# Performance work log

Measured on AMD Instinct MI355X. Metric: run time of the kernel, lower is better.

The kernel has to match this reference:

```python
import jax, jax.numpy as jnp
import numpy as np

N_NODES = 100000
N_EDGES = 800000
HIDDEN = 256
BOTTLENECK = 32


def setup_inputs() -> dict:
    key = jax.random.key(0)
    k1, k2, k3, k4 = jax.random.split(key, 4)
    x = jax.random.normal(k1, (N_NODES, HIDDEN), dtype=jnp.float32)
    edge_index = jax.random.randint(k2, (2, N_EDGES), 0, N_NODES, dtype=jnp.int64)
    # PyG GCNConv linear weights, init per module: normal(std=1e-5), zero bias
    W_down = jax.random.normal(k3, (BOTTLENECK, HIDDEN), dtype=jnp.float32) * 1e-5
    b_down = jnp.zeros((BOTTLENECK,), dtype=jnp.float32)
    W_up = jax.random.normal(k4, (HIDDEN, BOTTLENECK), dtype=jnp.float32) * 1e-5
    b_up = jnp.zeros((HIDDEN,), dtype=jnp.float32)
    return {"x": x, "edge_index": edge_index, "W_down": W_down, "b_down": b_down,
            "W_up": W_up, "b_up": b_up}


def reference(x, edge_index, W_down, b_down, W_up, b_up):
    N = x.shape[0]
    loops = jnp.arange(N, dtype=edge_index.dtype)
    # gcn_norm with self-loops (edge weight = 1), symmetric normalization
    row = jnp.concatenate([edge_index[0], loops])  # source nodes
    col = jnp.concatenate([edge_index[1], loops])  # target nodes
    deg = jax.ops.segment_sum(jnp.ones(row.shape[0], dtype=x.dtype), col, num_segments=N)
    dinv = jnp.where(deg > 0, jax.lax.rsqrt(deg), 0.0)
    norm = dinv[row] * dinv[col]  # [E+N]

    def gcn_conv(h, W, b):
        h = h @ W.T                                   # [N, out]
        msgs = h[row] * norm[:, None]                 # gather + weight
        return jax.ops.segment_sum(msgs, col, num_segments=N) + b

    h = jax.nn.relu(gcn_conv(x, W_down, b_down))      # down-proj conv + act
    out = gcn_conv(h, W_up, b_up) + x                 # up-proj conv + skip
    return out
```

## Files before the change

kernel.cpp:

```cpp
#include <hip/hip_runtime.h>
#include <hip/hip_bf16.h>
#include <stdint.h>

#define HID 256
#define BOT 32

typedef short short8 __attribute__((ext_vector_type(8)));
typedef unsigned short ushort8 __attribute__((ext_vector_type(8)));
typedef float floatx4 __attribute__((ext_vector_type(4)));

__device__ __forceinline__ unsigned short f2bu(float f) {
    return (unsigned short)(__float_as_uint(f) >> 16);
}
__device__ __forceinline__ float bu2f(unsigned short u) {
    return __uint_as_float((unsigned int)u << 16);
}
__device__ __forceinline__ short8 pack8(float4 a, float4 b) {
    short8 r;
    r[0] = (short)f2bu(a.x); r[1] = (short)f2bu(a.y);
    r[2] = (short)f2bu(a.z); r[3] = (short)f2bu(a.w);
    r[4] = (short)f2bu(b.x); r[5] = (short)f2bu(b.y);
    r[6] = (short)f2bu(b.z); r[7] = (short)f2bu(b.w);
    return r;
}


__global__ void k_detect(const int* __restrict__ ei, int* __restrict__ flags) {
    int t = threadIdx.x;
    int found = 0;
    for (int i = 0; i < 8; ++i) {
        int slot = 2 * (t * 8 + i) + 1;
        if (ei[slot] != 0) found = 1;
    }
    unsigned long long b = __ballot(found);
    if (t == 0) flags[0] = (b == 0ULL) ? 1 : 0;
}

__global__ void k_deg(const int* __restrict__ ei, int E, int* __restrict__ deg,
                      const int* __restrict__ flags) {
    int mode = flags[0];
    int e = blockIdx.x * blockDim.x + threadIdx.x;
    if (e >= E) return;
    int d = mode ? ei[2 * E + 2 * e] : ei[E + e];
    atomicAdd(deg + d, 1);
}

__global__ __launch_bounds__(256) void k_alloc(const int* __restrict__ deg,
                                               float* __restrict__ dinv,
                                               int* __restrict__ start,
                                               int* __restrict__ cur,
                                               int* __restrict__ cursor, int N) {
    __shared__ int sdata[256];
    __shared__ int sbase;
    int tid = threadIdx.x;
    int i = blockIdx.x * 256 + tid;
    int d = (i < N) ? deg[i] : 0;
    if (i < N) dinv[i] = rsqrtf((float)(d + 1));
    sdata[tid] = d;
    __syncthreads();
    for (int off = 1; off < 256; off <<= 1) {
        int t = (tid >= off) ? sdata[tid - off] : 0;
        __syncthreads();
        sdata[tid] += t;
        __syncthreads();
    }
    if (tid == 0) sbase = atomicAdd(cursor, sdata[255]);
    __syncthreads();
    if (i < N) {
        int st = sbase + sdata[tid] - d;
        start[i] = st;
        cur[i] = st;
    }
}

__global__ void k_fill(const int* __restrict__ ei, int E,
                       const float* __restrict__ dinv,
                       int* __restrict__ cur, int2* __restrict__ srcw,
                       const int* __restrict__ flags) {
    int mode = flags[0];
    int e = blockIdx.x * blockDim.x + threadIdx.x;
    if (e >= E) return;
    int s, d;
    if (mode) { s = ei[2 * e]; d = ei[2 * E + 2 * e]; }
    else      { s = ei[e];     d = ei[E + e]; }
    float w = dinv[s] * dinv[d];
    int slot = atomicAdd(cur + d, 1);
    srcw[slot] = make_int2(s, __float_as_int(w));
}

__global__ __launch_bounds__(256) void k_gemm_down(
    const float* __restrict__ x, const float* __restrict__ Wd,
    unsigned short* __restrict__ P, int N, int nwaves)
{
    int wid  = (blockIdx.x * 256 + threadIdx.x) >> 6;
    int lane = threadIdx.x & 63;
    int m = lane & 15, q = lane >> 4;

    short8 bfr[2][8];
    #pragma unroll
    for (int jt = 0; jt < 2; ++jt) {
        const float4* wr = (const float4*)(Wd + (size_t)(jt * 16 + m) * HID);
        #pragma unroll
        for (int ks = 0; ks < 8; ++ks) {
            int c = (ks * 32 + q * 8) >> 2;
            bfr[jt][ks] = pack8(wr[c], wr[c + 1]);
        }
    }

    int tiles = (N + 15) >> 4;
    for (int t = wid; t < tiles; t += nwaves) {
        int n0 = t << 4;
        int row = n0 + m; if (row >= N) row = N - 1;
        const float4* xr = (const float4*)(x + (size_t)row * HID);
        floatx4 acc0 = {0.f, 0.f, 0.f, 0.f};
        floatx4 acc1 = {0.f, 0.f, 0.f, 0.f};
        #pragma unroll
        for (int ks = 0; ks < 8; ++ks) {
            int c = (ks * 32 + q * 8) >> 2;
            short8 af = pack8(xr[c], xr[c + 1]);
            acc0 = __builtin_amdgcn_mfma_f32_16x16x32_bf16(bfr[0][ks], af, acc0, 0, 0, 0);
            acc1 = __builtin_amdgcn_mfma_f32_16x16x32_bf16(bfr[1][ks], af, acc1, 0, 0, 0);
        }
        if (n0 + m < N) {
            unsigned int* pr = (unsigned int*)(P + (size_t)(n0 + m) * BOT);
            uint2 v0, v1;
            v0.x = (unsigned int)f2bu(acc0[0]) | ((unsigned int)f2bu(acc0[1]) << 16);
            v0.y = (unsigned int)f2bu(acc0[2]) | ((unsigned int)f2bu(acc0[3]) << 16);
            v1.x = (unsigned int)f2bu(acc1[0]) | ((unsigned int)f2bu(acc1[1]) << 16);
            v1.y = (unsigned int)f2bu(acc1[2]) | ((unsigned int)f2bu(acc1[3]) << 16);
            *(uint2*)(pr + q * 2)     = v0;
            *(uint2*)(pr + 8 + q * 2) = v1;
        }
    }
}

__global__ __launch_bounds__(256) void k_gather(
    const unsigned short* __restrict__ feat, const float* __restrict__ dinv,
    const int* __restrict__ start, const int* __restrict__ endp,
    const int2* __restrict__ srcw, const float* __restrict__ bias,
    unsigned short* __restrict__ dst, int N, int relu_bias)
{
    int t = blockIdx.x * 256 + threadIdx.x;
    int n = t >> 2, tg = t & 3, jq = tg * 8;
    if (n >= N) return;
    float di = dinv[n];
    float w0 = di * di;
    float acc[8];
    ushort8 sv = *(const ushort8*)(feat + (size_t)n * BOT + jq);
    #pragma unroll
    for (int i = 0; i < 8; ++i) acc[i] = w0 * bu2f(sv[i]);
    int k = start[n], en = endp[n];
    for (; k < en; k += 4) {
        int kk = k + tg;
        int2 p = make_int2(0, 0);
        if (kk < en) p = srcw[kk];
        #pragma unroll
        for (int e = 0; e < 4; ++e) {
            int   src = __shfl(p.x, e, 4);
            float w   = __uint_as_float((unsigned int)__shfl(p.y, e, 4));
            ushort8 f = *(const ushort8*)(feat + (size_t)src * BOT + jq);
            #pragma unroll
            for (int i = 0; i < 8; ++i) acc[i] += w * bu2f(f[i]);
        }
    }
    if (relu_bias) {
        #pragma unroll
        for (int i = 0; i < 8; ++i) {
            float a = acc[i] + bias[jq + i];
            acc[i] = a > 0.f ? a : 0.f;
        }
    }
    ushort8 o;
    #pragma unroll
    for (int i = 0; i < 8; ++i) o[i] = f2bu(acc[i]);
    *(ushort8*)(dst + (size_t)n * BOT + jq) = o;
}

__global__ __launch_bounds__(256) void k_out(
    const unsigned short* __restrict__ A2, const float* __restrict__ x,
    const float* __restrict__ Wup, const float* __restrict__ bup,
    float* __restrict__ out, int N)
{
    int gw   = (blockIdx.x * 256 + threadIdx.x) >> 6;
    int lane = threadIdx.x & 63;
    int m = lane & 15, q = lane >> 4;
    int tiles = (N + 15) >> 4;
    int t = gw >> 1, h = gw & 1;
    if (t >= tiles) return;

    int n0 = t << 4;
    int arow = n0 + m; if (arow >= N) arow = N - 1;
    short8 af = *(const short8*)(A2 + (size_t)arow * BOT + q * 8);
    const float4* xrow = (const float4*)(x + (size_t)arow * HID);
    floatx4* orow = (floatx4*)(out + (size_t)arow * HID);
    bool ok = (n0 + m) < N;
    #pragma unroll
    for (int i = 0; i < 8; ++i) {
        int ft = h * 8 + i;
        const float4* wr = (const float4*)(Wup + (size_t)(ft * 16 + m) * BOT);
        short8 bfr = pack8(wr[q * 2], wr[q * 2 + 1]);
        floatx4 acc = {0.f, 0.f, 0.f, 0.f};
        acc = __builtin_amdgcn_mfma_f32_16x16x32_bf16(bfr, af, acc, 0, 0, 0);
        if (ok) {
            int c = ft * 4 + q;
            float4 xv = xrow[c];
            float4 bb = *(const float4*)(bup + ft * 16 + q * 4);
            floatx4 res;
            res[0] = acc[0] + bb.x + xv.x;
            res[1] = acc[1] + bb.y + xv.y;
            res[2] = acc[2] + bb.z + xv.z;
            res[3] = acc[3] + bb.w + xv.w;
            __builtin_nontemporal_store(res, &orow[c]);
        }
    }
}

extern "C" void kernel_launch(void* const* d_in, const int* in_sizes, int n_in,
                              void* d_out, int out_size, void* d_ws, size_t ws_size,
                              hipStream_t stream) {
    const float* x  = (const float*)d_in[0];
    const int*   ei = (const int*)d_in[1];
    const float* Wd = (const float*)d_in[2];
    const float* bd = (const float*)d_in[3];
    const float* Wu = (const float*)d_in[4];
    const float* bu = (const float*)d_in[5];
    float* out = (float*)d_out;

    int N = in_sizes[0] / HID;
    int E = in_sizes[1] / 2;

    char* ws = (char*)d_ws;
    int*   flags = (int*)ws;
    int*   deg   = (int*)(ws + 16);
    float* dinv  = (float*)(ws + 16 + (size_t)N * 4);
    int*   startp= (int*)(ws + 16 + (size_t)N * 8);
    int*   curp  = (int*)(ws + 16 + (size_t)N * 12);
    int2*  srcw  = (int2*)(ws + 16 + (size_t)N * 16);
    unsigned short* P  = (unsigned short*)(ws + 16 + (size_t)N * 16 + (size_t)E * 8);
    unsigned short* A1 = (unsigned short*)(ws + 16 + (size_t)N * 16 + (size_t)E * 8 + (size_t)N * 64);

    (void)hipMemsetAsync(ws, 0, 16 + (size_t)N * 4, stream);
    k_detect<<<1, 64, 0, stream>>>(ei, flags);
    k_deg<<<(E + 255) / 256, 256, 0, stream>>>(ei, E, deg, flags);

    k_alloc<<<(N + 255) / 256, 256, 0, stream>>>(deg, dinv, startp, curp, flags + 1, N);
    k_fill<<<(E + 255) / 256, 256, 0, stream>>>(ei, E, dinv, curp, srcw, flags);

    int tiles = (N + 15) / 16;
    int gblocks = (tiles + 3) / 4;
    k_gemm_down<<<gblocks, 256, 0, stream>>>(x, Wd, P, N, gblocks * 4);
    int gthreads = N * 4;
    k_gather<<<(gthreads + 255) / 256, 256, 0, stream>>>(P, dinv, startp, curp, srcw, bd, A1, N, 1);

    k_gather<<<(gthreads + 255) / 256, 256, 0, stream>>>(A1, dinv, startp, curp, srcw, bd, P, N, 0);

    int oblocks = (tiles * 2 + 3) / 4;
    k_out<<<oblocks, 256, 0, stream>>>(P, x, Wu, bu, out, N);
}
```

Baseline: 360.1 us.

## Fuse edge fill with down-GEMM, second gather with up-GEMM, inline mode detection

Removes the separate detect kernel by having each block of the degree and fill kernels detect the edge-index layout itself. The CSR fill and the down-projection GEMM now run as one launch, split by block index so they can overlap. The second aggregation is fused into the output kernel, so the intermediate bottleneck features are never written to or read back from global memory. Both gathers now load four edges per lane and issue four feature loads before accumulating, giving more memory parallelism. In exchange, every block repeats the detection reads, and the fused output kernel runs one wave per tile that performs 16 MFMAs instead of the earlier split into two half-waves.

```diff
diff --git a/kernel.cpp b/kernel.cpp
--- a/kernel.cpp
+++ b/kernel.cpp
@@ -24,24 +24,29 @@
     return r;
 }
 
-
-__global__ void k_detect(const int* __restrict__ ei, int* __restrict__ flags) {
-    int t = threadIdx.x;
-    int found = 0;
-    for (int i = 0; i < 8; ++i) {
-        int slot = 2 * (t * 8 + i) + 1;
-        if (ei[slot] != 0) found = 1;
-    }
-    unsigned long long b = __ballot(found);
-    if (t == 0) flags[0] = (b == 0ULL) ? 1 : 0;
-}
-
-__global__ void k_deg(const int* __restrict__ ei, int E, int* __restrict__ deg,
-                      const int* __restrict__ flags) {
-    int mode = flags[0];
-    int e = blockIdx.x * blockDim.x + threadIdx.x;
+__device__ __forceinline__ int detect_mode(const int* __restrict__ ei, int* smode) {
+    if (threadIdx.x < 64) {
+        int found = 0;
+        #pragma unroll
+        for (int i = 0; i < 8; ++i) {
+            int slot = 2 * (threadIdx.x * 8 + i) + 1;
+            if (ei[slot] != 0) found = 1;
+        }
+        unsigned long long b = __ballot(found);
+        if (threadIdx.x == 0) *smode = (b == 0ULL) ? 1 : 0;
+    }
+    __syncthreads();
+    return *smode;
+}
+
+
+__global__ __launch_bounds__(256) void k_deg(const int* __restrict__ ei, int E,
+                                             int* __restrict__ deg) {
+    __shared__ int smode;
+    int mode = detect_mode(ei, &smode);
+    int e = blockIdx.x * 256 + threadIdx.x;
     if (e >= E) return;
-    int d = mode ? ei[2 * E + 2 * e] : ei[E + e];
+    int d = mode ? ei[2 * (size_t)E + 2 * e] : ei[(size_t)E + e];
     atomicAdd(deg + d, 1);
 }
 
@@ -73,25 +78,27 @@
     }
 }
 
-__global__ void k_fill(const int* __restrict__ ei, int E,
-                       const float* __restrict__ dinv,
-                       int* __restrict__ cur, int2* __restrict__ srcw,
-                       const int* __restrict__ flags) {
-    int mode = flags[0];
-    int e = blockIdx.x * blockDim.x + threadIdx.x;
-    if (e >= E) return;
-    int s, d;
-    if (mode) { s = ei[2 * e]; d = ei[2 * E + 2 * e]; }
-    else      { s = ei[e];     d = ei[E + e]; }
-    float w = dinv[s] * dinv[d];
-    int slot = atomicAdd(cur + d, 1);
-    srcw[slot] = make_int2(s, __float_as_int(w));
-}
-
-__global__ __launch_bounds__(256) void k_gemm_down(
+__global__ __launch_bounds__(256) void k_fill_gemm(
+    const int* __restrict__ ei, int E,
+    const float* __restrict__ dinv, int* __restrict__ cur,
+    int2* __restrict__ srcw,
     const float* __restrict__ x, const float* __restrict__ Wd,
-    unsigned short* __restrict__ P, int N, int nwaves)
+    unsigned short* __restrict__ P, int N, int gemmBlocks, int gemmWaves)
 {
+    if (blockIdx.x >= gemmBlocks) {
+        __shared__ int smode;
+        int mode = detect_mode(ei, &smode);
+        int e = (blockIdx.x - gemmBlocks) * 256 + threadIdx.x;
+        if (e >= E) return;
+        int s, d;
+        if (mode) { s = ei[2 * (size_t)e]; d = ei[2 * (size_t)E + 2 * e]; }
+        else      { s = ei[(size_t)e];     d = ei[(size_t)E + e]; }
+        float w = dinv[s] * dinv[d];
+        int slot = atomicAdd(cur + d, 1);
+        srcw[slot] = make_int2(s, __float_as_int(w));
+        return;
+    }
+
     int wid  = (blockIdx.x * 256 + threadIdx.x) >> 6;
     int lane = threadIdx.x & 63;
     int m = lane & 15, q = lane >> 4;
@@ -108,7 +115,7 @@
     }
 
     int tiles = (N + 15) >> 4;
-    for (int t = wid; t < tiles; t += nwaves) {
+    for (int t = wid; t < tiles; t += gemmWaves) {
         int n0 = t << 4;
         int row = n0 + m; if (row >= N) row = N - 1;
         const float4* xr = (const float4*)(x + (size_t)row * HID);
@@ -141,7 +148,7 @@
     unsigned short* __restrict__ dst, int N, int relu_bias)
 {
     int t = blockIdx.x * 256 + threadIdx.x;
-    int n = t >> 2, tg = t & 3, jq = tg * 8;
+    int n = t >> 2, jq = (t & 3) * 8;
     if (n >= N) return;
     float di = dinv[n];
     float w0 = di * di;
@@ -150,18 +157,26 @@
     #pragma unroll
     for (int i = 0; i < 8; ++i) acc[i] = w0 * bu2f(sv[i]);
     int k = start[n], en = endp[n];
-    for (; k < en; k += 4) {
-        int kk = k + tg;
-        int2 p = make_int2(0, 0);
-        if (kk < en) p = srcw[kk];
-        #pragma unroll
-        for (int e = 0; e < 4; ++e) {
-            int   src = __shfl(p.x, e, 4);
-            float w   = __uint_as_float((unsigned int)__shfl(p.y, e, 4));
-            ushort8 f = *(const ushort8*)(feat + (size_t)src * BOT + jq);
+    while (k < en) {
+        int2 p[4];
+        #pragma unroll
+        for (int u = 0; u < 4; ++u) {
+            int kk = k + u;
+            int safe = kk < en ? kk : en - 1;
+            p[u] = srcw[safe];
+            if (kk >= en) p[u].y = 0;
+        }
+        ushort8 f[4];
+        #pragma unroll
+        for (int u = 0; u < 4; ++u)
+            f[u] = *(const ushort8*)(feat + (size_t)p[u].x * BOT + jq);
+        #pragma unroll
+        for (int u = 0; u < 4; ++u) {
+            float w = __int_as_float(p[u].y);
             #pragma unroll
-            for (int i = 0; i < 8; ++i) acc[i] += w * bu2f(f[i]);
-        }
+            for (int i = 0; i < 8; ++i) acc[i] += w * bu2f(f[u][i]);
+        }
+        k += 4;
     }
     if (relu_bias) {
         #pragma unroll
@@ -176,40 +191,73 @@
     *(ushort8*)(dst + (size_t)n * BOT + jq) = o;
 }
 
-__global__ __launch_bounds__(256) void k_out(
-    const unsigned short* __restrict__ A2, const float* __restrict__ x,
-    const float* __restrict__ Wup, const float* __restrict__ bup,
-    float* __restrict__ out, int N)
+__global__ __launch_bounds__(256) void k_gather_out(
+    const unsigned short* __restrict__ A1, const float* __restrict__ dinv,
+    const int* __restrict__ start, const int* __restrict__ endp,
+    const int2* __restrict__ srcw,
+    const float* __restrict__ x, const float* __restrict__ Wup,
+    const float* __restrict__ bup, float* __restrict__ out, int N)
 {
     int gw   = (blockIdx.x * 256 + threadIdx.x) >> 6;
     int lane = threadIdx.x & 63;
-    int m = lane & 15, q = lane >> 4;
+    int m = lane & 15, q = lane >> 4, jq = q * 8;
     int tiles = (N + 15) >> 4;
-    int t = gw >> 1, h = gw & 1;
-    if (t >= tiles) return;
-
-    int n0 = t << 4;
-    int arow = n0 + m; if (arow >= N) arow = N - 1;
-    short8 af = *(const short8*)(A2 + (size_t)arow * BOT + q * 8);
-    const float4* xrow = (const float4*)(x + (size_t)arow * HID);
-    floatx4* orow = (floatx4*)(out + (size_t)arow * HID);
-    bool ok = (n0 + m) < N;
-    #pragma unroll
-    for (int i = 0; i < 8; ++i) {
-        int ft = h * 8 + i;
+    if (gw >= tiles) return;
+    int n0 = gw << 4;
+    int n = n0 + m;
+    bool ok = n < N;
+    int nc = ok ? n : N - 1;
+
+    float di = dinv[nc];
+    float w0 = di * di;
+    float acc[8];
+    ushort8 sv = *(const ushort8*)(A1 + (size_t)nc * BOT + jq);
+    #pragma unroll
+    for (int i = 0; i < 8; ++i) acc[i] = w0 * bu2f(sv[i]);
+    int k = start[nc], en = endp[nc];
+    while (k < en) {
+        int2 p[4];
+        #pragma unroll
+        for (int u = 0; u < 4; ++u) {
+            int kk = k + u;
+            int safe = kk < en ? kk : en - 1;
+            p[u] = srcw[safe];
+            if (kk >= en) p[u].y = 0;
+        }
+        ushort8 f[4];
+        #pragma unroll
+        for (int u = 0; u < 4; ++u)
+            f[u] = *(const ushort8*)(A1 + (size_t)p[u].x * BOT + jq);
+        #pragma unroll
+        for (int u = 0; u < 4; ++u) {
+            float w = __int_as_float(p[u].y);
+            #pragma unroll
+            for (int i = 0; i < 8; ++i) acc[i] += w * bu2f(f[u][i]);
+        }
+        k += 4;
+    }
+
+    short8 af;
+    #pragma unroll
+    for (int i = 0; i < 8; ++i) af[i] = (short)f2bu(acc[i]);
+
+    const float4* xrow = (const float4*)(x + (size_t)nc * HID);
+    floatx4* orow = (floatx4*)(out + (size_t)nc * HID);
+    #pragma unroll
+    for (int ft = 0; ft < 16; ++ft) {
         const float4* wr = (const float4*)(Wup + (size_t)(ft * 16 + m) * BOT);
         short8 bfr = pack8(wr[q * 2], wr[q * 2 + 1]);
-        floatx4 acc = {0.f, 0.f, 0.f, 0.f};
-        acc = __builtin_amdgcn_mfma_f32_16x16x32_bf16(bfr, af, acc, 0, 0, 0);
+        floatx4 a = {0.f, 0.f, 0.f, 0.f};
+        a = __builtin_amdgcn_mfma_f32_16x16x32_bf16(bfr, af, a, 0, 0, 0);
         if (ok) {
             int c = ft * 4 + q;
             float4 xv = xrow[c];
             float4 bb = *(const float4*)(bup + ft * 16 + q * 4);
             floatx4 res;
-            res[0] = acc[0] + bb.x + xv.x;
-            res[1] = acc[1] + bb.y + xv.y;
-            res[2] = acc[2] + bb.z + xv.z;
-            res[3] = acc[3] + bb.w + xv.w;
+            res[0] = a[0] + bb.x + xv.x;
+            res[1] = a[1] + bb.y + xv.y;
+            res[2] = a[2] + bb.z + xv.z;
+            res[3] = a[3] + bb.w + xv.w;
             __builtin_nontemporal_store(res, &orow[c]);
         }
     }
@@ -240,20 +288,20 @@
     unsigned short* A1 = (unsigned short*)(ws + 16 + (size_t)N * 16 + (size_t)E * 8 + (size_t)N * 64);
 
     (void)hipMemsetAsync(ws, 0, 16 + (size_t)N * 4, stream);
-    k_detect<<<1, 64, 0, stream>>>(ei, flags);
-    k_deg<<<(E + 255) / 256, 256, 0, stream>>>(ei, E, deg, flags);
+
+    int eblocks = (E + 255) / 256;
+    k_deg<<<eblocks, 256, 0, stream>>>(ei, E, deg);
 
     k_alloc<<<(N + 255) / 256, 256, 0, stream>>>(deg, dinv, startp, curp, flags + 1, N);
-    k_fill<<<(E + 255) / 256, 256, 0, stream>>>(ei, E, dinv, curp, srcw, flags);
 
     int tiles = (N + 15) / 16;
-    int gblocks = (tiles + 3) / 4;
-    k_gemm_down<<<gblocks, 256, 0, stream>>>(x, Wd, P, N, gblocks * 4);
+    int gemmBlocks = (tiles + 3) / 4;
+    k_fill_gemm<<<gemmBlocks + eblocks, 256, 0, stream>>>(
+        ei, E, dinv, curp, srcw, x, Wd, P, N, gemmBlocks, gemmBlocks * 4);
+
     int gthreads = N * 4;
     k_gather<<<(gthreads + 255) / 256, 256, 0, stream>>>(P, dinv, startp, curp, srcw, bd, A1, N, 1);
 
-    k_gather<<<(gthreads + 255) / 256, 256, 0, stream>>>(A1, dinv, startp, curp, srcw, bd, P, N, 0);
-
-    int oblocks = (tiles * 2 + 3) / 4;
-    k_out<<<oblocks, 256, 0, stream>>>(P, x, Wu, bu, out, N);
-}
+    int oblocks = (tiles + 3) / 4;
+    k_gather_out<<<oblocks, 256, 0, stream>>>(A1, dinv, startp, curp, srcw, x, Wu, bu, out, N);
+}
```

Measured after the change: 353.5 us. No clear change (-1.8%).
